# Kernel optimization log

Hardware: AMD Instinct MI355X
Metric: run time of the kernel (lower is better)

Reference implementation:

```python
import jax, jax.numpy as jnp
import numpy as np

D = 1024   # feature_dim
K = 10     # num_anchors
B = 16384  # batch
H = 8      # num_heads


def setup_inputs() -> dict:
    key = jax.random.key(0)
    ks = jax.random.split(key, 12)
    f32 = jnp.float32

    def w(k, shape, scale=0.02):
        return (jax.random.normal(k, shape, f32) * scale)

    return {
        "features": jax.random.normal(ks[0], (B, D), f32),
        "anchors": w(ks[1], (K, D), 0.1),
        # anchor_refiner: Linear(D, D//2) -> ReLU -> Linear(D//2, D) -> Tanh
        "ar_w1": w(ks[2], (D, D // 2)), "ar_b1": jnp.zeros((D // 2,), f32),
        "ar_w2": w(ks[3], (D // 2, D)), "ar_b2": jnp.zeros((D,), f32),
        # attention projections
        "q_w": w(ks[4], (D, D)), "q_b": jnp.zeros((D,), f32),
        "k_w": w(ks[5], (D, D)), "k_b": jnp.zeros((D,), f32),
        "v_w": w(ks[6], (D, D)), "v_b": jnp.zeros((D,), f32),
        "o_w": w(ks[7], (D, D)), "o_b": jnp.zeros((D,), f32),
        # feature_enhancer: LayerNorm -> Linear(D,2D) -> GELU -> Linear(2D,D)
        "ln_g": jnp.ones((D,), f32), "ln_b": jnp.zeros((D,), f32),
        "ff_w1": w(ks[8], (D, 2 * D)), "ff_b1": jnp.zeros((2 * D,), f32),
        "ff_w2": w(ks[9], (2 * D, D)), "ff_b2": jnp.zeros((D,), f32),
        "div_w": jnp.asarray(0.001, f32),
        "cen_w": jnp.asarray(0.001, f32),
    }


def _l2norm(x, eps=1e-8):
    n = jnp.linalg.norm(x, axis=-1, keepdims=True)
    return x / jnp.maximum(n, eps)


def _layernorm(x, g, b, eps=1e-5):
    mu = jnp.mean(x, axis=-1, keepdims=True)
    var = jnp.mean(jnp.square(x - mu), axis=-1, keepdims=True)
    return (x - mu) * jax.lax.rsqrt(var + eps) * g + b


def reference(features, anchors, ar_w1, ar_b1, ar_w2, ar_b2,
              q_w, q_b, k_w, k_b, v_w, v_b, o_w, o_b,
              ln_g, ln_b, ff_w1, ff_b1, ff_w2, ff_b2, div_w, cen_w):
    b = features.shape[0]
    hd = D // H
    fn = _l2norm(features)                                 # [B, D]

    # anchor refinement
    refin = jnp.tanh(jax.nn.relu(anchors @ ar_w1 + ar_b1) @ ar_w2 + ar_b2)
    an = _l2norm(anchors + 0.1 * refin)                    # [K, D]

    # multi-head cross-attention to anchors
    q = (fn @ q_w + q_b).reshape(b, H, hd)                 # [B, H, hd]
    k = (an @ k_w + k_b).reshape(K, H, hd)                 # [K, H, hd]
    v = (an @ v_w + v_b).reshape(K, H, hd)
    scores = jnp.einsum('bhd,khd->bhk', q, k) / jnp.sqrt(jnp.asarray(hd, fn.dtype))
    aw = jax.nn.softmax(scores, axis=-1)                   # [B, H, K]
    att = jnp.einsum('bhk,khd->bhd', aw, v).reshape(b, D)
    att = att @ o_w + o_b

    # feature enhancer (dropout inactive: eval mode)
    enh = fn + 0.1 * att
    h = jax.nn.gelu(_layernorm(enh, ln_g, ln_b) @ ff_w1 + ff_b1, approximate=False)
    enh = h @ ff_w2 + ff_b2
    final = fn + 0.2 * enh                                 # [B, D]

    # diversity loss: pdist over K=10 anchors (45 pairs)
    diff = an[:, None, :] - an[None, :, :]                 # [K, K, D]
    dmat = jnp.sqrt(jnp.maximum(jnp.sum(diff * diff, -1), 1e-24))
    iu = np.triu_indices(K, 1)
    div_loss = jnp.exp(-jnp.maximum(dmat[iu].mean(), 1e-6))

    # center loss: attention-weighted feature-anchor distances
    avg_att = aw.mean(axis=1)                              # [B, K]
    sq = (jnp.sum(fn * fn, 1, keepdims=True) + jnp.sum(an * an, 1)
          - 2.0 * fn @ an.T)
    fa_dist = jnp.sqrt(jnp.maximum(sq, 1e-12))             # [B, K]
    center_loss = jnp.sum(avg_att * fa_dist, axis=1).mean()

    geo = jnp.abs(div_w) * div_loss + jnp.abs(cen_w) * center_loss
    geo = jnp.clip(geo, 0.0, 0.01)
    return final, geo
```

## Files before the change

kernel.cpp:

```cpp
#include <hip/hip_runtime.h>
#include <hip/hip_bf16.h>
#include <math.h>

typedef __hip_bfloat16 bf16;

#define D_  1024
#define K_  10
#define B_  16384
#define H_  8
#define HD_ 128

struct alignas(16) BF8 { bf16 v[8]; };
struct alignas(8)  BF4 { bf16 v[4]; };

typedef __bf16 bf8v __attribute__((ext_vector_type(8)));
typedef float  f4v  __attribute__((ext_vector_type(4)));

__device__ __forceinline__ float b2f(bf16 x){ return __bfloat162float(x); }
__device__ __forceinline__ bf16  f2b(float x){ return __float2bfloat16(x); }

#define GL2LDS16(g, l) __builtin_amdgcn_global_load_lds( \
    (__attribute__((address_space(1))) void*)(g), \
    (__attribute__((address_space(3))) void*)(l), 16, 0, 0)

__global__ __launch_bounds__(256) void l2norm_k(const float* __restrict__ x,
                                                bf16* __restrict__ fnb) {
  int b = blockIdx.x, t = threadIdx.x;
  float4 v = ((const float4*)(x + (size_t)b * D_))[t];
  float p = v.x*v.x + v.y*v.y + v.z*v.z + v.w*v.w;
  #pragma unroll
  for (int o = 32; o > 0; o >>= 1) p += __shfl_down(p, o);
  __shared__ float wsum[4];
  if ((t & 63) == 0) wsum[t >> 6] = p;
  __syncthreads();
  __shared__ float inv_s;
  if (t == 0) inv_s = 1.f / fmaxf(sqrtf(wsum[0]+wsum[1]+wsum[2]+wsum[3]), 1e-8f);
  __syncthreads();
  float iv = inv_s;
  BF4 o;
  o.v[0] = f2b(v.x*iv); o.v[1] = f2b(v.y*iv);
  o.v[2] = f2b(v.z*iv); o.v[3] = f2b(v.w*iv);
  ((BF4*)(fnb + (size_t)b * D_))[t] = o;
}

__global__ __launch_bounds__(256) void wt_k(const float* __restrict__ w,
                                            bf16* __restrict__ wt, int R, int C) {
  __shared__ float tle[32][33];
  int c0 = blockIdx.x * 32, r0 = blockIdx.y * 32;
  int tx = threadIdx.x & 31, ty = threadIdx.x >> 5;
  #pragma unroll
  for (int i = 0; i < 32; i += 8)
    tle[ty + i][tx] = w[(size_t)(r0 + ty + i) * C + c0 + tx];
  __syncthreads();
  #pragma unroll
  for (int i = 0; i < 32; i += 8)
    wt[(size_t)(c0 + ty + i) * R + r0 + tx] = f2b(tle[tx][ty + i]);
}

template<int COLS, int KD, int ACT>
__global__ __launch_bounds__(256) void panelmm_k(
    const float* __restrict__ A, const float* __restrict__ W,
    const float* __restrict__ bias, const float* __restrict__ aux,
    float* __restrict__ out,
    const float* __restrict__ W2, const float* __restrict__ bias2,
    float* __restrict__ out2, int N, int npanel) {
  constexpr int GROUPS = 256 / COLS;
  constexpr int DCH = KD / GROUPS;
  __shared__ float A_s[K_][KD];
  __shared__ float part[K_][COLS][GROUPS];
  const int t = threadIdx.x;
  int blk = blockIdx.x;
  const float* Wm = W; const float* bm = bias; float* om = out;
  if (blk >= npanel) { blk -= npanel; Wm = W2; bm = bias2; om = out2; }
  const int panel = blk;
  for (int i = t; i < K_*KD; i += 256) A_s[0][i] = A[i];
  __syncthreads();
  const int cg = t % COLS, g = t / COLS;
  const int col = panel*COLS + cg;
  float s[K_];
  #pragma unroll
  for (int r = 0; r < K_; ++r) s[r] = 0.f;
  const float* wp = Wm + (size_t)(g*DCH)*N + col;
  for (int d = g*DCH; d < (g+1)*DCH; ++d) {
    float wv = *wp; wp += N;
    #pragma unroll
    for (int r = 0; r < K_; ++r) s[r] = fmaf(A_s[r][d], wv, s[r]);
  }
  #pragma unroll
  for (int r = 0; r < K_; ++r) part[r][cg][g] = s[r];
  __syncthreads();
  for (int o = t; o < K_*COLS; o += 256) {
    int r = o / COLS, c = o % COLS;
    float v = 0.f;
    #pragma unroll
    for (int gg = 0; gg < GROUPS; ++gg) v += part[r][c][gg];
    v += bm[panel*COLS + c];
    if constexpr (ACT == 1) v = fmaxf(v, 0.f);
    if constexpr (ACT == 2) v = aux[(size_t)r*N + panel*COLS + c] + 0.1f*tanhf(v);
    om[(size_t)r*N + panel*COLS + c] = v;
  }
}

template<int TRANSOUT, typename TW>
__global__ __launch_bounds__(256) void smallmm_k(
    const float* __restrict__ A, const TW* __restrict__ W,
    bf16* __restrict__ outb, float scale) {
  constexpr int COLS = 64, GROUPS = 4, DCH = 32, NW = 1024;
  __shared__ float A_s[K_][128];
  __shared__ float part[K_][COLS][GROUPS];
  const int t = threadIdx.x;
  const int h = blockIdx.x & 7, panel = blockIdx.x >> 3;
  for (int i = t; i < K_*128; i += 256) {
    int r = i >> 7, j = i & 127;
    A_s[r][j] = A[r*1024 + h*128 + j];
  }
  __syncthreads();
  const int cg = t % COLS, g = t / COLS;
  const int col = panel*COLS + cg;
  float s[K_];
  #pragma unroll
  for (int r = 0; r < K_; ++r) s[r] = 0.f;
  const TW* wp = W + (size_t)(h*128 + g*DCH)*NW + col;
  for (int d = g*DCH; d < g*DCH + DCH; ++d) {
    float wv;
    if constexpr (sizeof(TW) == 2) wv = b2f(*wp); else wv = *wp;
    wp += NW;
    #pragma unroll
    for (int r = 0; r < K_; ++r) s[r] = fmaf(A_s[r][d], wv, s[r]);
  }
  #pragma unroll
  for (int r = 0; r < K_; ++r) part[r][cg][g] = s[r];
  __syncthreads();
  for (int o = t; o < 16*COLS; o += 256) {
    int r = o / COLS, c = o % COLS;
    float v = 0.f;
    if (r < K_) {
      #pragma unroll
      for (int gg = 0; gg < GROUPS; ++gg) v += part[r][c][gg];
      v *= scale;
    }
    if constexpr (TRANSOUT) outb[(size_t)(panel*COLS + c)*128 + h*16 + r] = f2b(v);
    else                    outb[(size_t)(h*16 + r)*NW + panel*COLS + c] = f2b(v);
  }
}

__global__ void sbias_k(const float* __restrict__ qb, const float* __restrict__ Km,
                        const float* __restrict__ na, float* __restrict__ sb) {
  int c = threadIdx.x;
  if (c < 128) {
    int h = c >> 4, k = c & 15;
    float s = 0.f;
    if (k < K_) {
      for (int j = 0; j < HD_; ++j)
        s = fmaf(qb[h*HD_ + j], Km[(size_t)k*D_ + h*HD_ + j], s);
    }
    sb[c] = s * 0.08838834764831845f;
  } else {
    int j = c - 128;
    sb[c] = (j < K_) ? (1.f + na[j]) : 0.f;
  }
}

__global__ __launch_bounds__(256) void anext_k(const float* __restrict__ an,
                                               bf16* __restrict__ wt) {
  int k = blockIdx.x;
  bf16* dst = wt + (size_t)(128 + k) * 1024;
  int i = threadIdx.x * 4;
  BF4 o;
  if (k < K_) {
    float4 a = *(const float4*)(an + (size_t)k*1024 + i);
    o.v[0] = f2b(-2.f*a.x); o.v[1] = f2b(-2.f*a.y);
    o.v[2] = f2b(-2.f*a.z); o.v[3] = f2b(-2.f*a.w);
  } else {
    o.v[0] = o.v[1] = o.v[2] = o.v[3] = f2b(0.f);
  }
  *(BF4*)(dst + i) = o;
}

__global__ __launch_bounds__(256) void ar3_k(const float* __restrict__ an_un,
    float* __restrict__ an, float* __restrict__ na, float* __restrict__ divloss) {
  __shared__ float a_s[K_][D_];
  __shared__ float nrm[K_];
  __shared__ float dm[45];
  const int t = threadIdx.x;
  for (int i = t; i < K_*D_; i += 256) a_s[0][i] = an_un[i];
  __syncthreads();
  const int wid = t >> 6, lane = t & 63;
  for (int r = wid; r < K_; r += 4) {
    float p = 0.f;
    for (int j = lane; j < D_; j += 64) p += a_s[r][j]*a_s[r][j];
    #pragma unroll
    for (int o = 1; o < 64; o <<= 1) p += __shfl_xor(p, o);
    if (lane == 0) nrm[r] = p;
  }
  __syncthreads();
  for (int i = t; i < K_*D_; i += 256) {
    int r = i >> 10;
    float iv = 1.f / fmaxf(sqrtf(nrm[r]), 1e-8f);
    float v = a_s[0][i] * iv;
    a_s[0][i] = v;
    an[i] = v;
  }
  if (t < K_) {
    float iv = 1.f / fmaxf(sqrtf(nrm[t]), 1e-8f);
    na[t] = nrm[t] * iv * iv;
  }
  __syncthreads();
  const int pr = t >> 2, sub = t & 3;
  if (pr < 45) {
    int i = 0, j = 0, c = pr;
    for (i = 0; i < K_; ++i) { int cnt = K_-1-i; if (c < cnt) { j = i+1+c; break; } c -= cnt; }
    float s = 0.f;
    for (int d = sub*256; d < sub*256 + 256; ++d) {
      float df = a_s[i][d] - a_s[j][d]; s += df*df;
    }
    s += __shfl_xor(s, 1); s += __shfl_xor(s, 2);
    if (sub == 0) dm[pr] = sqrtf(fmaxf(s, 1e-24f));
  }
  __syncthreads();
  if (t == 0) {
    float m = 0.f;
    for (int p = 0; p < 45; ++p) m += dm[p];
    m *= (1.f/45.f);
    *divloss = expf(-fmaxf(m, 1e-6f));
  }
}

template<int EPI, typename TO>
__global__ __launch_bounds__(256) void mgemm_k(
    const bf16* __restrict__ A, const bf16* __restrict__ Bt,
    const float* __restrict__ bias, const bf16* __restrict__ aux,
    TO* __restrict__ out, int M, int N, int Kd, float scale) {
  constexpr int BM = 128, BN = 128, BK = 32;
  __shared__ bf16 As[BM][BK];
  __shared__ bf16 Bs[BN][BK];
  const int tid = threadIdx.x;
  const int nMB = M / BM;
  const int nwg = gridDim.x;
  int wg = blockIdx.x;
  wg = (wg & 7) * (nwg >> 3) + (wg >> 3);
  const int mb = wg % nMB, nb = wg / nMB;
  const int bm = mb * BM, bn = nb * BN;

  const int srow = tid >> 2;
  const int sk   = (tid & 3) * 8;
  const bf16* ga = A  + (size_t)(bm + srow) * Kd + sk;
  const bf16* gb = Bt + (size_t)(bn + srow) * Kd + sk;
  const size_t rstep = (size_t)64 * Kd;
  bf16* la = &As[0][0] + tid * 8;
  bf16* lb = &Bs[0][0] + tid * 8;

  const int w    = tid >> 6;
  const int lane = tid & 63;
  const int wr = (w >> 1) * 64, wc = (w & 1) * 64;
  const int fr = lane & 15, fg = lane >> 4;

  f4v acc[4][4];
  const f4v zz = {0.f, 0.f, 0.f, 0.f};
  #pragma unroll
  for (int m = 0; m < 4; ++m)
    #pragma unroll
    for (int n = 0; n < 4; ++n) acc[m][n] = zz;

  for (int k0 = 0; k0 < Kd; k0 += BK) {
    GL2LDS16(ga,         la);
    GL2LDS16(ga + rstep, la + 2048);
    GL2LDS16(gb,         lb);
    GL2LDS16(gb + rstep, lb + 2048);
    __syncthreads();
    bf8v af[4], bf_[4];
    #pragma unroll
    for (int m = 0; m < 4; ++m)
      af[m] = *(const bf8v*)&As[wr + m*16 + fr][fg*8];
    #pragma unroll
    for (int n = 0; n < 4; ++n)
      bf_[n] = *(const bf8v*)&Bs[wc + n*16 + fr][fg*8];
    #pragma unroll
    for (int m = 0; m < 4; ++m)
      #pragma unroll
      for (int n = 0; n < 4; ++n)
        acc[m][n] = __builtin_amdgcn_mfma_f32_16x16x32_bf16(af[m], bf_[n], acc[m][n], 0, 0, 0);
    __syncthreads();
    ga += BK; gb += BK;
  }

  float bv[4];
  #pragma unroll
  for (int n = 0; n < 4; ++n) bv[n] = bias[bn + wc + n*16 + fr];
  #pragma unroll
  for (int m = 0; m < 4; ++m) {
    #pragma unroll
    for (int r = 0; r < 4; ++r) {
      const int row = bm + wr + m*16 + fg*4 + r;
      #pragma unroll
      for (int n = 0; n < 4; ++n) {
        const int col = bn + wc + n*16 + fr;
        float x = acc[m][n][r] + bv[n];
        if constexpr (EPI == 1) x = b2f(aux[(size_t)row * N + col]) + scale * x;
        if constexpr (EPI == 2) x = 0.5f * x * (1.f + erff(x * 0.70710678118654752f));
        if constexpr (sizeof(TO) == 2) out[(size_t)row * N + col] = f2b(x);
        else                           out[(size_t)row * N + col] = x;
      }
    }
  }
}

template<int EPI, typename TO>
__global__ __launch_bounds__(512, 2) void mgemm256_k(
    const bf16* __restrict__ A, const bf16* __restrict__ Bt,
    const float* __restrict__ bias, const bf16* __restrict__ aux,
    TO* __restrict__ out, int M, int N, int Kd, float scale) {
  constexpr int BM = 256, BN = 256, BK = 32, DEPTH = 4;
  __shared__ bf16 As[DEPTH][BM*BK];
  __shared__ bf16 Bs[DEPTH][BN*BK];
  const int tid = threadIdx.x;
  const int nMB = M / BM;
  const int nwg = gridDim.x;
  int wg = blockIdx.x;
  wg = (wg & 7) * (nwg >> 3) + (wg >> 3);
  const int bm = (wg % nMB) * BM, bn = (wg / nMB) * BN;

  const int sr = tid >> 2, ss = tid & 3;
  const int sx = ((ss ^ (sr & 3)) * 8);
  const bf16* gA0 = A  + (size_t)(bm + sr)       * Kd + sx;
  const bf16* gA1 = A  + (size_t)(bm + sr + 128) * Kd + sx;
  const bf16* gB0 = Bt + (size_t)(bn + sr)       * Kd + sx;
  const bf16* gB1 = Bt + (size_t)(bn + sr + 128) * Kd + sx;

  const int wid = tid >> 6, lane = tid & 63;
  const int wm = wid >> 2, wn = wid & 3;
  const int fr = lane & 15, fg = lane >> 4;
  const int rslot = (fg ^ (fr & 3)) * 8;

  f4v acc[8][4];
  const f4v zz = {0.f, 0.f, 0.f, 0.f};
  #pragma unroll
  for (int m = 0; m < 8; ++m)
    #pragma unroll
    for (int n = 0; n < 4; ++n) acc[m][n] = zz;

  const int nt = Kd / BK;
  #pragma unroll
  for (int p = 0; p < DEPTH-1; ++p) {
    if (p < nt) {
      const int ko = p * BK;
      GL2LDS16(gA0 + ko, &As[p][0] + tid*8);
      GL2LDS16(gA1 + ko, &As[p][0] + tid*8 + 4096);
      GL2LDS16(gB0 + ko, &Bs[p][0] + tid*8);
      GL2LDS16(gB1 + ko, &Bs[p][0] + tid*8 + 4096);
    }
  }

  for (int t = 0; t < nt; ++t) {
    const int rem = nt - 1 - t;
    if (rem >= 2)      asm volatile("s_waitcnt vmcnt(8)" ::: "memory");
    else if (rem == 1) asm volatile("s_waitcnt vmcnt(4)" ::: "memory");
    else               asm volatile("s_waitcnt vmcnt(0)" ::: "memory");
    __builtin_amdgcn_sched_barrier(0);
    __builtin_amdgcn_s_barrier();
    __builtin_amdgcn_sched_barrier(0);
    if (t + DEPTH - 1 < nt) {
      const int st = t + DEPTH - 1;
      const int sl = st & (DEPTH-1);
      const int ko = st * BK;
      GL2LDS16(gA0 + ko, &As[sl][0] + tid*8);
      GL2LDS16(gA1 + ko, &As[sl][0] + tid*8 + 4096);
      GL2LDS16(gB0 + ko, &Bs[sl][0] + tid*8);
      GL2LDS16(gB1 + ko, &Bs[sl][0] + tid*8 + 4096);
    }
    const int slot = t & (DEPTH-1);
    const bf16* la = &As[slot][0];
    const bf16* lb = &Bs[slot][0];
    bf8v af[8], bq[4];
    #pragma unroll
    for (int m = 0; m < 4; ++m)
      af[m] = *(const bf8v*)(la + (wm*128 + m*16 + fr)*BK + rslot);
    #pragma unroll
    for (int n = 0; n < 4; ++n)
      bq[n] = *(const bf8v*)(lb + (wn*64 + n*16 + fr)*BK + rslot);
    __builtin_amdgcn_sched_barrier(0);
    #pragma unroll
    for (int m = 4; m < 8; ++m)
      af[m] = *(const bf8v*)(la + (wm*128 + m*16 + fr)*BK + rslot);
    asm volatile("s_waitcnt lgkmcnt(4)" ::: "memory");
    __builtin_amdgcn_sched_barrier(0);
    __builtin_amdgcn_s_setprio(1);
    #pragma unroll
    for (int m = 0; m < 4; ++m)
      #pragma unroll
      for (int n = 0; n < 4; ++n)
        acc[m][n] = __builtin_amdgcn_mfma_f32_16x16x32_bf16(af[m], bq[n], acc[m][n], 0, 0, 0);
    asm volatile("s_waitcnt lgkmcnt(0)" ::: "memory");
    __builtin_amdgcn_sched_barrier(0);
    #pragma unroll
    for (int m = 4; m < 8; ++m)
      #pragma unroll
      for (int n = 0; n < 4; ++n)
        acc[m][n] = __builtin_amdgcn_mfma_f32_16x16x32_bf16(af[m], bq[n], acc[m][n], 0, 0, 0);
    __builtin_amdgcn_s_setprio(0);
  }

  float bv[4];
  #pragma unroll
  for (int n = 0; n < 4; ++n) bv[n] = bias[bn + wn*64 + n*16 + fr];
  #pragma unroll
  for (int m = 0; m < 8; ++m) {
    #pragma unroll
    for (int r = 0; r < 4; ++r) {
      const int row = bm + wm*128 + m*16 + fg*4 + r;
      #pragma unroll
      for (int n = 0; n < 4; ++n) {
        const int col = bn + wn*64 + n*16 + fr;
        float x = acc[m][n][r] + bv[n];
        if constexpr (EPI == 1) x = b2f(aux[(size_t)row * N + col]) + scale * x;
        if constexpr (EPI == 2) x = 0.5f * x * (1.f + erff(x * 0.70710678118654752f));
        if constexpr (sizeof(TO) == 2) out[(size_t)row * N + col] = f2b(x);
        else                           out[(size_t)row * N + col] = x;
      }
    }
  }
}

__global__ __launch_bounds__(256) void attn2_k(
    const float* __restrict__ S, bf16* __restrict__ awp,
    float* __restrict__ cen_acc) {
  __shared__ float cred[4];
  const int t = threadIdx.x;
  const int wid = t >> 6, lane = t & 63;
  const int sub = lane & 7, head = lane >> 3;
  const int k0 = sub*2, k1 = k0 + 1;
  float c_acc = 0.f;
  const int row0 = blockIdx.x * 32 + wid * 8;

  for (int i = 0; i < 8; ++i) {
    const int row = row0 + i;
    const float* Sr = S + (size_t)row * 256;
    float2 sv = *(const float2*)(Sr + head*16 + k0);
    float v0 = (k0 < K_) ? sv.x : -1e30f;
    float v1 = (k1 < K_) ? sv.y : -1e30f;
    float m = fmaxf(v0, v1);
    m = fmaxf(m, __shfl_xor(m,1)); m = fmaxf(m, __shfl_xor(m,2)); m = fmaxf(m, __shfl_xor(m,4));
    float e0 = (k0 < K_) ? __expf(v0 - m) : 0.f;
    float e1 = (k1 < K_) ? __expf(v1 - m) : 0.f;
    float es = e0 + e1;
    es += __shfl_xor(es,1); es += __shfl_xor(es,2); es += __shfl_xor(es,4);
    float inv = 1.f / es;
    float a0 = e0 * inv, a1 = e1 * inv;
    bf16 b0 = f2b(a0), b1 = f2b(a1);
    unsigned int pk = (unsigned int)(*(unsigned short*)&b0)
                    | ((unsigned int)(*(unsigned short*)&b1) << 16);
    *(unsigned int*)(awp + (size_t)row*128 + head*16 + k0) = pk;
    float g0 = a0, g1 = a1;
    g0 += __shfl_xor(g0,8); g0 += __shfl_xor(g0,16); g0 += __shfl_xor(g0,32);
    g1 += __shfl_xor(g1,8); g1 += __shfl_xor(g1,16); g1 += __shfl_xor(g1,32);
    if (sub < 5) {
      float d20 = Sr[128 + k0];
      float d21 = Sr[128 + k1];
      c_acc = fmaf(g0, sqrtf(fmaxf(d20, 1e-12f)), c_acc);
      c_acc = fmaf(g1, sqrtf(fmaxf(d21, 1e-12f)), c_acc);
    }
  }
  #pragma unroll
  for (int o = 1; o < 64; o <<= 1) c_acc += __shfl_xor(c_acc, o);
  if (lane == 0) cred[wid] = c_acc;
  __syncthreads();
  if (t == 0) {
    float s = (cred[0]+cred[1]+cred[2]+cred[3]) * (1.f/64.f/(float)B_);
    atomicAdd(cen_acc, s);
  }
}

__global__ __launch_bounds__(256) void ln_k(const bf16* __restrict__ x,
    const float* __restrict__ g, const float* __restrict__ bta,
    bf16* __restrict__ out) {
  int b = blockIdx.x, t = threadIdx.x;
  BF4 ld = ((const BF4*)(x + (size_t)b * D_))[t];
  float v[4];
  #pragma unroll
  for (int j = 0; j < 4; ++j) v[j] = b2f(ld.v[j]);
  float s = v[0]+v[1]+v[2]+v[3];
  #pragma unroll
  for (int o = 32; o > 0; o >>= 1) s += __shfl_down(s, o);
  __shared__ float w1[4], w2[4];
  if ((t & 63) == 0) w1[t >> 6] = s;
  __syncthreads();
  __shared__ float mu_s, rs_s;
  if (t == 0) mu_s = (w1[0]+w1[1]+w1[2]+w1[3]) * (1.f/D_);
  __syncthreads();
  float mu = mu_s;
  float qv = 0.f;
  #pragma unroll
  for (int j = 0; j < 4; ++j) { float d = v[j]-mu; qv += d*d; }
  #pragma unroll
  for (int o = 32; o > 0; o >>= 1) qv += __shfl_down(qv, o);
  if ((t & 63) == 0) w2[t >> 6] = qv;
  __syncthreads();
  if (t == 0) rs_s = rsqrtf((w2[0]+w2[1]+w2[2]+w2[3]) * (1.f/D_) + 1e-5f);
  __syncthreads();
  float rs = rs_s;
  BF4 o;
  #pragma unroll
  for (int j = 0; j < 4; ++j) {
    int col = t*4 + j;
    o.v[j] = f2b((v[j]-mu)*rs*g[col] + bta[col]);
  }
  ((BF4*)(out + (size_t)b * D_))[t] = o;
}

__global__ void geo_k(const float* __restrict__ divl, const float* __restrict__ cen,
                      const float* __restrict__ div_w, const float* __restrict__ cen_w,
                      float* __restrict__ out) {
  float g = fabsf(*div_w) * (*divl) + fabsf(*cen_w) * (*cen);
  out[0] = fminf(fmaxf(g, 0.f), 0.01f);
}

extern "C" void kernel_launch(void* const* d_in, const int* in_sizes, int n_in,
                              void* d_out, int out_size, void* d_ws, size_t ws_size,
                              hipStream_t stream) {
  const float* features = (const float*)d_in[0];
  const float* anchors  = (const float*)d_in[1];
  const float* ar_w1 = (const float*)d_in[2];
  const float* ar_b1 = (const float*)d_in[3];
  const float* ar_w2 = (const float*)d_in[4];
  const float* ar_b2 = (const float*)d_in[5];
  const float* q_w = (const float*)d_in[6];
  const float* q_b = (const float*)d_in[7];
  const float* k_w = (const float*)d_in[8];
  const float* k_b = (const float*)d_in[9];
  const float* v_w = (const float*)d_in[10];
  const float* v_b = (const float*)d_in[11];
  const float* o_w = (const float*)d_in[12];
  const float* o_b = (const float*)d_in[13];
  const float* ln_g = (const float*)d_in[14];
  const float* ln_b = (const float*)d_in[15];
  const float* ff_w1 = (const float*)d_in[16];
  const float* ff_b1 = (const float*)d_in[17];
  const float* ff_w2 = (const float*)d_in[18];
  const float* ff_b2 = (const float*)d_in[19];
  const float* div_w = (const float*)d_in[20];
  const float* cen_w = (const float*)d_in[21];
  float* out = (float*)d_out;

  char* w = (char*)d_ws;
  bf16* ws_fnb = (bf16*)w;  w += (size_t)B_ * D_ * 2;
  bf16* ws_enh = (bf16*)w;  w += (size_t)B_ * D_ * 2;
  bf16* ws_ln  = (bf16*)w;  w += (size_t)B_ * D_ * 2;
  bf16* ws_h   = (bf16*)w;  w += (size_t)B_ * 2048 * 2;
  float* ws_S  = (float*)w; w += (size_t)B_ * 256 * 4;
  bf16* ws_awp = (bf16*)w;  w += (size_t)B_ * 128 * 2;
  bf16* ws_wq  = (bf16*)w;  w += (size_t)D_ * D_ * 2;
  bf16* ws_w1t = (bf16*)w;  w += (size_t)D_ * 2048 * 2;
  bf16* ws_w2t = (bf16*)w;  w += (size_t)2048 * D_ * 2;
  bf16* ws_wt  = (bf16*)w;  w += (size_t)256 * D_ * 2;
  bf16* ws_vt  = (bf16*)w;  w += (size_t)D_ * 128 * 2;
  float* ws_har = (float*)w;  w += (size_t)K_ * (D_/2) * 4;
  float* ws_anu = (float*)w;  w += (size_t)K_ * D_ * 4;
  float* ws_an  = (float*)w;  w += (size_t)K_ * D_ * 4;
  float* ws_k   = (float*)w;  w += (size_t)K_ * D_ * 4;
  float* ws_v   = (float*)w;  w += (size_t)K_ * D_ * 4;
  float* ws_na  = (float*)w;  w += 256;
  float* ws_div = (float*)w;  w += 256;
  float* ws_cen = (float*)w;  w += 256;
  float* ws_sb  = (float*)w;  w += 512;
  if ((size_t)(w - (char*)d_ws) > ws_size) return;

  hipMemsetAsync(ws_cen, 0, 4, stream);

  wt_k<<<dim3(D_/32,   D_/32),   256, 0, stream>>>(q_w,   ws_wq,  D_,   D_);
  wt_k<<<dim3(2048/32, D_/32),   256, 0, stream>>>(ff_w1, ws_w1t, D_,   2048);
  wt_k<<<dim3(D_/32,   2048/32), 256, 0, stream>>>(ff_w2, ws_w2t, 2048, D_);

  l2norm_k<<<B_, 256, 0, stream>>>(features, ws_fnb);

  panelmm_k<32, 1024, 1><<<16, 256, 0, stream>>>(
      anchors, ar_w1, ar_b1, nullptr, ws_har,
      nullptr, nullptr, nullptr, D_/2, 16);
  panelmm_k<64, 512, 2><<<16, 256, 0, stream>>>(
      ws_har, ar_w2, ar_b2, anchors, ws_anu,
      nullptr, nullptr, nullptr, D_, 16);
  ar3_k<<<1, 256, 0, stream>>>(ws_anu, ws_an, ws_na, ws_div);
  panelmm_k<64, 1024, 0><<<32, 256, 0, stream>>>(
      ws_an, k_w, k_b, nullptr, ws_k,
      v_w, v_b, ws_v, D_, 16);

  smallmm_k<0, bf16><<<128, 256, 0, stream>>>(ws_k, ws_wq, ws_wt, 0.08838834764831845f);
  anext_k<<<128, 256, 0, stream>>>(ws_an, ws_wt);
  sbias_k<<<1, 256, 0, stream>>>(q_b, ws_k, ws_na, ws_sb);
  smallmm_k<1, float><<<128, 256, 0, stream>>>(ws_v, o_w, ws_vt, 1.f);

  mgemm_k<0, float><<<dim3((B_/128)*(256/128)), 256, 0, stream>>>(
      ws_fnb, ws_wt, ws_sb, nullptr, ws_S, B_, 256, D_, 0.f);

  attn2_k<<<B_/32, 256, 0, stream>>>(ws_S, ws_awp, ws_cen);

  mgemm256_k<1, bf16><<<dim3((B_/256)*(D_/256)), 512, 0, stream>>>(
      ws_awp, ws_vt, o_b, ws_fnb, ws_enh, B_, D_, 128, 0.1f);

  ln_k<<<B_, 256, 0, stream>>>(ws_enh, ln_g, ln_b, ws_ln);

  mgemm256_k<2, bf16><<<dim3((B_/256)*(2048/256)), 512, 0, stream>>>(
      ws_ln, ws_w1t, ff_b1, nullptr, ws_h, B_, 2048, D_, 0.f);

  mgemm256_k<1, float><<<dim3((B_/256)*(D_/256)), 512, 0, stream>>>(
      ws_h, ws_w2t, ff_b2, ws_fnb, out, B_, D_, 2048, 0.2f);

  geo_k<<<1, 1, 0, stream>>>(ws_div, ws_cen, div_w, cen_w, out + (size_t)B_ * D_);
}
```

Measured before the change: 464.9 us.

## Switch 256x256 GEMM to BK=64 double-buffered pipeline with XOR swizzle

Replaces the 4-deep BK=32 LDS pipeline with a 2-stage double buffer at BK=64. It uses a new 8-way XOR swizzle for the 128-byte rows and plain __syncthreads instead of hand-tuned vmcnt/lgkmcnt waits. The goal is fewer barriers and loop iterations per K, with twice as many MFMAs per iteration. In exchange it loses the deeper prefetch, drops the 2-blocks-per-CU occupancy hint, and the compiler now has to schedule LDS reads interleaved with MFMAs.

```diff
diff --git a/kernel.cpp b/kernel.cpp
--- a/kernel.cpp
+++ b/kernel.cpp
@@ -306,13 +306,13 @@
 }
 
 template<int EPI, typename TO>
-__global__ __launch_bounds__(512, 2) void mgemm256_k(
+__global__ __launch_bounds__(512) void mgemm256_k(
     const bf16* __restrict__ A, const bf16* __restrict__ Bt,
     const float* __restrict__ bias, const bf16* __restrict__ aux,
     TO* __restrict__ out, int M, int N, int Kd, float scale) {
-  constexpr int BM = 256, BN = 256, BK = 32, DEPTH = 4;
-  __shared__ bf16 As[DEPTH][BM*BK];
-  __shared__ bf16 Bs[DEPTH][BN*BK];
+  constexpr int BM = 256, BN = 256, BK = 64;
+  __shared__ bf16 As[2][BM*BK];
+  __shared__ bf16 Bs[2][BN*BK];
   const int tid = threadIdx.x;
   const int nMB = M / BM;
   const int nwg = gridDim.x;
@@ -320,17 +320,16 @@
   wg = (wg & 7) * (nwg >> 3) + (wg >> 3);
   const int bm = (wg % nMB) * BM, bn = (wg / nMB) * BN;
 
-  const int sr = tid >> 2, ss = tid & 3;
-  const int sx = ((ss ^ (sr & 3)) * 8);
-  const bf16* gA0 = A  + (size_t)(bm + sr)       * Kd + sx;
-  const bf16* gA1 = A  + (size_t)(bm + sr + 128) * Kd + sx;
-  const bf16* gB0 = Bt + (size_t)(bn + sr)       * Kd + sx;
-  const bf16* gB1 = Bt + (size_t)(bn + sr + 128) * Kd + sx;
+  const int srow = tid >> 3;
+  const int scsw = ((tid & 7) ^ (srow & 7)) * 8;
+  const bf16* gA = A  + (size_t)(bm + srow) * Kd + scsw;
+  const bf16* gB = Bt + (size_t)(bn + srow) * Kd + scsw;
+  const size_t lstep = (size_t)64 * Kd;
 
   const int wid = tid >> 6, lane = tid & 63;
   const int wm = wid >> 2, wn = wid & 3;
   const int fr = lane & 15, fg = lane >> 4;
-  const int rslot = (fg ^ (fr & 3)) * 8;
+  const int fsw = fr & 7;
 
   f4v acc[8][4];
   const f4v zz = {0.f, 0.f, 0.f, 0.f};
@@ -340,64 +339,48 @@
     for (int n = 0; n < 4; ++n) acc[m][n] = zz;
 
   const int nt = Kd / BK;
-  #pragma unroll
-  for (int p = 0; p < DEPTH-1; ++p) {
-    if (p < nt) {
-      const int ko = p * BK;
-      GL2LDS16(gA0 + ko, &As[p][0] + tid*8);
-      GL2LDS16(gA1 + ko, &As[p][0] + tid*8 + 4096);
-      GL2LDS16(gB0 + ko, &Bs[p][0] + tid*8);
-      GL2LDS16(gB1 + ko, &Bs[p][0] + tid*8 + 4096);
-    }
-  }
-
+
+  #pragma unroll
+  for (int l = 0; l < 4; ++l) {
+    GL2LDS16(gA + l*lstep, &As[0][0] + tid*8 + l*4096);
+    GL2LDS16(gB + l*lstep, &Bs[0][0] + tid*8 + l*4096);
+  }
+  __syncthreads();
+
+  int buf = 0;
   for (int t = 0; t < nt; ++t) {
-    const int rem = nt - 1 - t;
-    if (rem >= 2)      asm volatile("s_waitcnt vmcnt(8)" ::: "memory");
-    else if (rem == 1) asm volatile("s_waitcnt vmcnt(4)" ::: "memory");
-    else               asm volatile("s_waitcnt vmcnt(0)" ::: "memory");
-    __builtin_amdgcn_sched_barrier(0);
-    __builtin_amdgcn_s_barrier();
-    __builtin_amdgcn_sched_barrier(0);
-    if (t + DEPTH - 1 < nt) {
-      const int st = t + DEPTH - 1;
-      const int sl = st & (DEPTH-1);
-      const int ko = st * BK;
-      GL2LDS16(gA0 + ko, &As[sl][0] + tid*8);
-      GL2LDS16(gA1 + ko, &As[sl][0] + tid*8 + 4096);
-      GL2LDS16(gB0 + ko, &Bs[sl][0] + tid*8);
-      GL2LDS16(gB1 + ko, &Bs[sl][0] + tid*8 + 4096);
-    }
-    const int slot = t & (DEPTH-1);
-    const bf16* la = &As[slot][0];
-    const bf16* lb = &Bs[slot][0];
-    bf8v af[8], bq[4];
-    #pragma unroll
-    for (int m = 0; m < 4; ++m)
-      af[m] = *(const bf8v*)(la + (wm*128 + m*16 + fr)*BK + rslot);
-    #pragma unroll
-    for (int n = 0; n < 4; ++n)
-      bq[n] = *(const bf8v*)(lb + (wn*64 + n*16 + fr)*BK + rslot);
-    __builtin_amdgcn_sched_barrier(0);
-    #pragma unroll
-    for (int m = 4; m < 8; ++m)
-      af[m] = *(const bf8v*)(la + (wm*128 + m*16 + fr)*BK + rslot);
-    asm volatile("s_waitcnt lgkmcnt(4)" ::: "memory");
-    __builtin_amdgcn_sched_barrier(0);
+    if (t + 1 < nt) {
+      const int ko = (t + 1) * BK;
+      #pragma unroll
+      for (int l = 0; l < 4; ++l) {
+        GL2LDS16(gA + l*lstep + ko, &As[buf^1][0] + tid*8 + l*4096);
+        GL2LDS16(gB + l*lstep + ko, &Bs[buf^1][0] + tid*8 + l*4096);
+      }
+    }
+    const bf16* la = &As[buf][0];
+    const bf16* lb = &Bs[buf][0];
+    bf8v bq[8];
+    #pragma unroll
+    for (int n = 0; n < 4; ++n) {
+      const int rb = wn*64 + n*16 + fr;
+      bq[n*2]   = *(const bf8v*)(lb + rb*64 + ((fg     ^ fsw) * 8));
+      bq[n*2+1] = *(const bf8v*)(lb + rb*64 + (((4+fg) ^ fsw) * 8));
+    }
     __builtin_amdgcn_s_setprio(1);
     #pragma unroll
-    for (int m = 0; m < 4; ++m)
+    for (int m = 0; m < 8; ++m) {
+      const int ra = wm*128 + m*16 + fr;
+      bf8v a0 = *(const bf8v*)(la + ra*64 + ((fg     ^ fsw) * 8));
+      bf8v a1 = *(const bf8v*)(la + ra*64 + (((4+fg) ^ fsw) * 8));
       #pragma unroll
-      for (int n = 0; n < 4; ++n)
-        acc[m][n] = __builtin_amdgcn_mfma_f32_16x16x32_bf16(af[m], bq[n], acc[m][n], 0, 0, 0);
-    asm volatile("s_waitcnt lgkmcnt(0)" ::: "memory");
-    __builtin_amdgcn_sched_barrier(0);
-    #pragma unroll
-    for (int m = 4; m < 8; ++m)
-      #pragma unroll
-      for (int n = 0; n < 4; ++n)
-        acc[m][n] = __builtin_amdgcn_mfma_f32_16x16x32_bf16(af[m], bq[n], acc[m][n], 0, 0, 0);
+      for (int n = 0; n < 4; ++n) {
+        acc[m][n] = __builtin_amdgcn_mfma_f32_16x16x32_bf16(a0, bq[n*2],   acc[m][n], 0, 0, 0);
+        acc[m][n] = __builtin_amdgcn_mfma_f32_16x16x32_bf16(a1, bq[n*2+1], acc[m][n], 0, 0, 0);
+      }
+    }
     __builtin_amdgcn_s_setprio(0);
+    __syncthreads();
+    buf ^= 1;
   }
 
   float bv[4];
```

Measured after the change: 420.0 us. 1.11x faster.
